# Optimization experiments

Measured on AMD Instinct MI355X. Metric: run time of the kernel, lower is better.

## Reference

```python
import jax, jax.numpy as jnp
import numpy as np

B, T, H, NCLS = 1024, 128, 512, 10
EMB, NDIG = 2, 3  # hard-coded in the torch module


def setup_inputs() -> dict:
    key = jax.random.key(0)
    ks = jax.random.split(key, 8)
    # kaiming_normal_ for a (fan_out, fan_in) matrix: std = sqrt(2/fan_in)
    def kaiming(k, shape):
        fan_in = shape[-1]
        return jax.random.normal(k, shape, dtype=jnp.float32) * np.sqrt(2.0 / fan_in)
    x = jax.random.randint(ks[0], (B, T), 0, NDIG)
    emb = jax.random.normal(ks[1], (NDIG, EMB), dtype=jnp.float32)
    # gate weights stacked in order (g, i, f, o) -> one fused GEMM per step
    Wx = jnp.concatenate([kaiming(ks[2 + j], (H, EMB)) for j in range(4)], axis=0)  # (4H, 2)
    kh = jax.random.split(ks[6], 4)
    Wh = jnp.concatenate([kaiming(kh[j], (H, H)) for j in range(4)], axis=0)  # (4H, H)
    b = jnp.zeros((4 * H,), dtype=jnp.float32)
    kp = jax.random.split(ks[7], 1)[0]
    Wp = kaiming(kp, (NCLS, H)).T  # stored transposed, as in the torch code
    bp = jnp.zeros((NCLS,), dtype=jnp.float32)
    return {"x": x, "emb": emb, "Wx": Wx, "Wh": Wh, "b": b, "Wp": Wp, "bp": bp}


def reference(x, emb, Wx, Wh, b, Wp, bp):
    # x: (B, T) int indices; emb: (3, 2); Wx: (4H, 2); Wh: (4H, H); b: (4H,)
    Bsz = x.shape[0]
    Hdim = Wh.shape[1]
    xe = emb[x]                                   # (B, T, 2) embedding lookup
    # precompute input projections for all timesteps (dim_x is tiny)
    gx_all = jnp.einsum('bte,ge->tbg', xe, Wx) + b  # (T, B, 4H)

    def step(carry, gx):
        h, c = carry
        z = gx + h @ Wh.T                         # (B, 4H) fused gate pre-activations
        g, i, f, o = jnp.split(z, 4, axis=-1)
        g = jnp.tanh(g)
        i = jax.nn.sigmoid(i)
        f = jax.nn.sigmoid(f)
        o = jax.nn.sigmoid(o)
        c = g * i + c * f
        h = jnp.tanh(c) * o
        return (h, c), None

    h0 = jnp.zeros((Bsz, Hdim), dtype=emb.dtype)
    c0 = jnp.zeros((Bsz, Hdim), dtype=emb.dtype)
    (h, _), _ = jax.lax.scan(step, (h0, c0), gx_all)
    p = h @ Wp + bp                               # only the last timestep's p is used
    return jax.nn.log_softmax(p, axis=-1)
```

## Files before the change

### kernel.cpp

```cpp
#include <hip/hip_runtime.h>
#include <math.h>

#define Bsz  1024
#define Tlen 128
#define Hdim 512
#define NCLS 10
#define NDIG 3
#define G4   2048

typedef short s8v __attribute__((ext_vector_type(8)));
typedef float f16v __attribute__((ext_vector_type(16)));

#define W6_OFF  0
#define GXD_OFF (2*1024*1024)
#define LL_OFF  (GXD_OFF + 32*1024)
#define LLF_OFF (LL_OFF + 4*1024*1024)
#define LLBUF   262144ull
#define WS_FAST_NEED ((size_t)LLF_OFF + 4*1024*1024)

static __device__ __forceinline__ unsigned short f2bf(float f) {
    unsigned int u = __float_as_uint(f);
    u = (u + 0x7FFFu + ((u >> 16) & 1u)) >> 16;
    return (unsigned short)u;
}
static __device__ __forceinline__ float bf2f(unsigned short s) {
    return __uint_as_float(((unsigned int)s) << 16);
}
static __device__ __forceinline__ s8v u2s(uint4 v) {
    union { uint4 u; s8v s; } x; x.u = v; return x.s;
}

__global__ __launch_bounds__(256) void prep_w6(const float* __restrict__ Wh,
                                               unsigned short* __restrict__ W6) {
    int idx = blockIdx.x * 256 + threadIdx.x;
    int l  = idx & 63;
    int c  = idx >> 6;
    int ks = c & 31, wn = c >> 5;
    int n  = wn * 32 + (l & 31);
    int jp = n >> 2, g = n & 3;
    int row = g * Hdim + jp;
    int kb  = ks * 16 + (l >> 5) * 8;
    const float* src = &Wh[(size_t)row * Hdim + kb];
    unsigned int p0 = f2bf(src[0]) | ((unsigned int)f2bf(src[1]) << 16);
    unsigned int p1 = f2bf(src[2]) | ((unsigned int)f2bf(src[3]) << 16);
    unsigned int p2 = f2bf(src[4]) | ((unsigned int)f2bf(src[5]) << 16);
    unsigned int p3 = f2bf(src[6]) | ((unsigned int)f2bf(src[7]) << 16);
    ((uint4*)W6)[idx] = make_uint4(p0, p1, p2, p3);
}

__global__ __launch_bounds__(256) void prep_gxd(const float* __restrict__ emb,
                                                const float* __restrict__ Wx,
                                                const float* __restrict__ b,
                                                float* __restrict__ gxd) {
    int idx = blockIdx.x * 256 + threadIdx.x;
    if (idx >= NDIG * G4) return;
    int col = idx % G4;
    int d   = idx / G4;
    int jp  = col >> 2;
    int g   = col & 3;
    int row = g * Hdim + jp;
    gxd[idx] = emb[d * 2 + 0] * Wx[row * 2 + 0]
             + emb[d * 2 + 1] * Wx[row * 2 + 1]
             + b[row];
}

__global__ __launch_bounds__(256) void zero_state(float4* __restrict__ p, int n4) {
    int i = blockIdx.x * 256 + threadIdx.x;
    if (i < n4) p[i] = make_float4(0.f, 0.f, 0.f, 0.f);
}

static __device__ __forceinline__ int slow_round(
    const unsigned long long* lr, unsigned int* hl, unsigned int want)
{
    unsigned long long g[16];
#pragma unroll
    for (int i = 0; i < 16; i++)
        g[i] = __hip_atomic_load(lr + i * 64, __ATOMIC_RELAXED,
                                 __HIP_MEMORY_SCOPE_AGENT);
    int ok = 1;
#pragma unroll
    for (int i = 0; i < 16; i++)
        ok &= ((unsigned int)(g[i] >> 32) == want) ? 1 : 0;
    if (!__all(ok)) return 0;
#pragma unroll
    for (int i = 0; i < 16; i++) hl[i * 64] = (unsigned int)g[i];
    return 1;
}

static __device__ __forceinline__ int try_fast(
    const unsigned long long* lr, unsigned int* hl, unsigned int want,
    int rounds)
{
    const unsigned long long* lrb = lr + 512;
    for (int r = 0; r < rounds; ++r) {
        unsigned long long g0,g1,g2,g3,g4,g5,g6,g7,g8,g9,g10,g11,g12,g13,g14,g15;
        asm volatile(
            "global_load_dwordx2 %[g0],  %[a], off sc0\n\t"
            "global_load_dwordx2 %[g1],  %[a], off offset:512 sc0\n\t"
            "global_load_dwordx2 %[g2],  %[a], off offset:1024 sc0\n\t"
            "global_load_dwordx2 %[g3],  %[a], off offset:1536 sc0\n\t"
            "global_load_dwordx2 %[g4],  %[a], off offset:2048 sc0\n\t"
            "global_load_dwordx2 %[g5],  %[a], off offset:2560 sc0\n\t"
            "global_load_dwordx2 %[g6],  %[a], off offset:3072 sc0\n\t"
            "global_load_dwordx2 %[g7],  %[a], off offset:3584 sc0\n\t"
            "global_load_dwordx2 %[g8],  %[b], off sc0\n\t"
            "global_load_dwordx2 %[g9],  %[b], off offset:512 sc0\n\t"
            "global_load_dwordx2 %[g10], %[b], off offset:1024 sc0\n\t"
            "global_load_dwordx2 %[g11], %[b], off offset:1536 sc0\n\t"
            "global_load_dwordx2 %[g12], %[b], off offset:2048 sc0\n\t"
            "global_load_dwordx2 %[g13], %[b], off offset:2560 sc0\n\t"
            "global_load_dwordx2 %[g14], %[b], off offset:3072 sc0\n\t"
            "global_load_dwordx2 %[g15], %[b], off offset:3584 sc0\n\t"
            "s_waitcnt vmcnt(0)"
            : [g0]"=&v"(g0),[g1]"=&v"(g1),[g2]"=&v"(g2),[g3]"=&v"(g3),
              [g4]"=&v"(g4),[g5]"=&v"(g5),[g6]"=&v"(g6),[g7]"=&v"(g7),
              [g8]"=&v"(g8),[g9]"=&v"(g9),[g10]"=&v"(g10),[g11]"=&v"(g11),
              [g12]"=&v"(g12),[g13]"=&v"(g13),[g14]"=&v"(g14),[g15]"=&v"(g15)
            : [a]"v"(lr), [b]"v"(lrb)
            : "memory");
        int ok = ((unsigned int)(g0  >> 32) == want) & ((unsigned int)(g1  >> 32) == want)
               & ((unsigned int)(g2  >> 32) == want) & ((unsigned int)(g3  >> 32) == want)
               & ((unsigned int)(g4  >> 32) == want) & ((unsigned int)(g5  >> 32) == want)
               & ((unsigned int)(g6  >> 32) == want) & ((unsigned int)(g7  >> 32) == want)
               & ((unsigned int)(g8  >> 32) == want) & ((unsigned int)(g9  >> 32) == want)
               & ((unsigned int)(g10 >> 32) == want) & ((unsigned int)(g11 >> 32) == want)
               & ((unsigned int)(g12 >> 32) == want) & ((unsigned int)(g13 >> 32) == want)
               & ((unsigned int)(g14 >> 32) == want) & ((unsigned int)(g15 >> 32) == want);
        if (__all(ok)) {
            hl[0*64]=(unsigned int)g0;   hl[1*64]=(unsigned int)g1;
            hl[2*64]=(unsigned int)g2;   hl[3*64]=(unsigned int)g3;
            hl[4*64]=(unsigned int)g4;   hl[5*64]=(unsigned int)g5;
            hl[6*64]=(unsigned int)g6;   hl[7*64]=(unsigned int)g7;
            hl[8*64]=(unsigned int)g8;   hl[9*64]=(unsigned int)g9;
            hl[10*64]=(unsigned int)g10; hl[11*64]=(unsigned int)g11;
            hl[12*64]=(unsigned int)g12; hl[13*64]=(unsigned int)g13;
            hl[14*64]=(unsigned int)g14; hl[15*64]=(unsigned int)g15;
            return 1;
        }
        if (r >= 2) __builtin_amdgcn_s_sleep(1);
    }
    return 0;
}

static __device__ __forceinline__ void stage_slice(
    const unsigned long long* fl, const unsigned long long* sl,
    unsigned int* hl, unsigned int want, int fasten, int burst)
{
    if (fasten && try_fast(fl, hl, want, burst)) return;
    for (;;) {
        if (slow_round(sl, hl, want)) return;
        if (fasten && try_fast(fl, hl, want, 1)) return;
        __builtin_amdgcn_s_sleep(1);
    }
}

__global__ __launch_bounds__(512, 2) void lstm_persist(
    const uint4* __restrict__ W6, const float* __restrict__ gxd,
    const int* __restrict__ x, unsigned long long* __restrict__ ll,
    unsigned long long* __restrict__ llf, int fasten,
    const float* __restrict__ Wp, const float* __restrict__ bp,
    float* __restrict__ out)
{
    __shared__ uint4 h_lds[2][2048];
    __shared__ float gxd_s[NDIG * G4];
    __shared__ int   x_s[4096];

    const int tid  = threadIdx.x;
    const int w    = tid >> 6;
    const int lane = tid & 63;
    const int hi   = lane >> 5;
    const int bl   = lane & 31;
    const int mt   = blockIdx.x & 31;
    const int nt   = blockIdx.x >> 5;

    s8v wfrag[32];
    {
        const uint4* wq = W6 + (size_t)((nt * 8 + w) * 32) * 64 + lane;
#pragma unroll
        for (int ks = 0; ks < 32; ks++) wfrag[ks] = u2s(wq[ks * 64]);
    }
    for (int i = tid; i < 4096; i += 512) {
        int b2 = i & 31, tt = i >> 5;
        x_s[tt * 32 + b2] = x[(mt * 32 + b2) * Tlen + tt];
    }
    for (int i = tid; i < NDIG * G4; i += 512) gxd_s[i] = gxd[i];
    __syncthreads();

    float c0 = 0.f, c1 = 0.f, c2 = 0.f, c3 = 0.f;
    const int jbase = nt * 64 + w * 8 + hi;
    const int q = (nt * 4 + (w >> 1)) * 64 + (w & 1) * 32 + bl;
    unsigned long long*       llst  = ll  + (size_t)mt * 8192 + q * 4 + hi * 2;
    unsigned long long*       llstf = llf + (size_t)mt * 8192 + q * 4 + hi * 2;
    const unsigned long long* llld  = ll  + (size_t)mt * 8192 + w * 1024 + lane;
    const unsigned long long* llfld = llf + (size_t)mt * 8192 + w * 1024 + lane;
    unsigned int* hlb = (unsigned int*)h_lds;

#pragma unroll 1
    for (int t = 0; t < Tlen; t++) {
        const int par = t & 1;

        stage_slice(llfld + (size_t)par * LLBUF, llld + (size_t)par * LLBUF,
                    hlb + par * 8192 + w * 1024 + lane, (unsigned int)t,
                    fasten, 8);
        __syncthreads();

        f16v acc = {0,0,0,0,0,0,0,0,0,0,0,0,0,0,0,0};
        const uint4* hb = &h_lds[par][0];
#pragma unroll
        for (int ks = 0; ks < 32; ks++) {
            s8v hf = u2s(hb[ks * 64 + lane]);
            acc = __builtin_amdgcn_mfma_f32_32x32x16_bf16(wfrag[ks], hf, acc,
                                                          0, 0, 0);
        }

        {
            int d = x_s[t * 32 + bl];
            float cc[4] = {c0, c1, c2, c3};
            unsigned short hh[4];
#pragma unroll
            for (int u = 0; u < 4; u++) {
                int jp = jbase + 2 * u;
                float4 g4 = *(const float4*)&gxd_s[d * G4 + jp * 4];
                float zg = acc[4*u+0] + g4.x;
                float zi = acc[4*u+1] + g4.y;
                float zf = acc[4*u+2] + g4.z;
                float zo = acc[4*u+3] + g4.w;
                float gv = 1.f - 2.f / (__expf(2.f * zg) + 1.f);
                float iv = 1.f / (1.f + __expf(-zi));
                float fv = 1.f / (1.f + __expf(-zf));
                float ov = 1.f / (1.f + __expf(-zo));
                float cn = gv * iv + cc[u] * fv;
                cc[u] = cn;
                hh[u] = f2bf((1.f - 2.f / (__expf(2.f * cn) + 1.f)) * ov);
            }
            c0 = cc[0]; c1 = cc[1]; c2 = cc[2]; c3 = cc[3];
            unsigned int p01 = (unsigned int)hh[0] | ((unsigned int)hh[1] << 16);
            unsigned int p23 = (unsigned int)hh[2] | ((unsigned int)hh[3] << 16);
            unsigned int q01 = __shfl_xor(p01, 32);
            unsigned int q23 = __shfl_xor(p23, 32);
            unsigned int lo2, hi2;
            if (hi == 0) {
                lo2 = (p01 & 0xffffu) | ((q01 & 0xffffu) << 16);
                hi2 = (p01 >> 16) | (q01 & 0xffff0000u);
            } else {
                lo2 = (q23 & 0xffffu) | ((p23 & 0xffffu) << 16);
                hi2 = (q23 >> 16) | (p23 & 0xffff0000u);
            }
            const unsigned long long tg =
                ((unsigned long long)(unsigned int)(t + 1)) << 32;
            const unsigned long long v0 = (unsigned long long)lo2 | tg;
            const unsigned long long v1 = (unsigned long long)hi2 | tg;
            const size_t pofs = (size_t)((t + 1) & 1) * LLBUF;
            if (fasten) {
                unsigned long long* fw = llstf + pofs;
                fw[0] = v0;
                fw[1] = v1;
            }
            unsigned long long* lw = llst + pofs;
            __hip_atomic_store(lw,     v0, __ATOMIC_RELAXED,
                               __HIP_MEMORY_SCOPE_AGENT);
            __hip_atomic_store(lw + 1, v1, __ATOMIC_RELAXED,
                               __HIP_MEMORY_SCOPE_AGENT);
        }
    }

    if (nt != 0) return;
    stage_slice(llfld, llld, hlb + w * 1024 + lane, (unsigned int)Tlen,
                fasten, 32);
    __syncthreads();
    float* wp_s = gxd_s;
    for (int i = tid; i < Hdim * NCLS; i += 512) wp_s[i] = Wp[i];
    __syncthreads();

#pragma unroll
    for (int rr = 0; rr < 4; rr++) {
        int blr = w * 4 + rr;
        int b   = mt * 32 + blr;
        uint4 hq = h_lds[0][(lane >> 1) * 64 + (lane & 1) * 32 + blr];
        union { uint4 u; unsigned short s[8]; } hu; hu.u = hq;
        float a[NCLS];
#pragma unroll
        for (int c = 0; c < NCLS; c++) a[c] = 0.f;
#pragma unroll
        for (int j = 0; j < 8; j++) {
            int k = lane * 8 + j;
            float hvv = bf2f(hu.s[j]);
#pragma unroll
            for (int c = 0; c < NCLS; c++) a[c] += hvv * wp_s[k * NCLS + c];
        }
#pragma unroll
        for (int off = 32; off > 0; off >>= 1) {
#pragma unroll
            for (int c = 0; c < NCLS; c++) a[c] += __shfl_down(a[c], off);
        }
        if (lane == 0) {
            float p[NCLS], m = -1e30f;
#pragma unroll
            for (int c = 0; c < NCLS; c++) { p[c] = a[c] + bp[c]; m = fmaxf(m, p[c]); }
            float s = 0.f;
#pragma unroll
            for (int c = 0; c < NCLS; c++) s += __expf(p[c] - m);
            float lse = m + logf(s);
#pragma unroll
            for (int c = 0; c < NCLS; c++) out[b * NCLS + c] = p[c] - lse;
        }
    }
}

extern "C" void kernel_launch(void* const* d_in, const int* in_sizes, int n_in,
                              void* d_out, int out_size, void* d_ws, size_t ws_size,
                              hipStream_t stream) {
    const int*   x   = (const int*)d_in[0];
    const float* emb = (const float*)d_in[1];
    const float* Wx  = (const float*)d_in[2];
    const float* Wh  = (const float*)d_in[3];
    const float* b   = (const float*)d_in[4];
    const float* Wp  = (const float*)d_in[5];
    const float* bp  = (const float*)d_in[6];
    float* out = (float*)d_out;
    char*  ws  = (char*)d_ws;

    int fasten = (ws_size >= WS_FAST_NEED) ? 1 : 0;

    unsigned short*     W6  = (unsigned short*)(ws + W6_OFF);
    float*              gxd = (float*)(ws + GXD_OFF);
    unsigned long long* ll  = (unsigned long long*)(ws + LL_OFF);
    unsigned long long* llf = (unsigned long long*)(ws + (fasten ? LLF_OFF
                                                                 : LL_OFF));

    prep_w6<<<512, 256, 0, stream>>>(Wh, W6);
    prep_gxd<<<(NDIG * G4 + 255) / 256, 256, 0, stream>>>(emb, Wx, b, gxd);
    {
        int nbytes = (fasten ? 8 : 4) * 1024 * 1024;
        int n4 = nbytes / 16;
        zero_state<<<(n4 + 255) / 256, 256, 0, stream>>>(
            (float4*)(ws + LL_OFF), n4);
    }

    void* args[] = { (void*)&W6, (void*)&gxd, (void*)&x, (void*)&ll,
                     (void*)&llf, (void*)&fasten,
                     (void*)&Wp, (void*)&bp, (void*)&out };
    hipLaunchCooperativeKernel((void*)lstm_persist, dim3(256), dim3(512),
                               args, 0, stream);
}
```

Baseline: 637.4 us.

## Add per-block sentinel flags to poll before reading fast h-exchange buffers

Adds a small sentinel array in the workspace. After writing its h slice to the fast buffer, each producer block waits for its stores to drain, runs a block barrier, and has thread 0 publish the step number. Consumers poll one sentinel word per producer before reading the full tagged slice, so they stop repeatedly loading the whole buffer. The cost is an extra vmcnt wait and __syncthreads per step on the producer side, plus the risk that sentinel visibility comes later than the data, which adds latency to the serial recurrence.

```diff
diff --git a/kernel.cpp b/kernel.cpp
--- a/kernel.cpp
+++ b/kernel.cpp
@@ -15,8 +15,9 @@
 #define GXD_OFF (2*1024*1024)
 #define LL_OFF  (GXD_OFF + 32*1024)
 #define LLF_OFF (LL_OFF + 4*1024*1024)
+#define SENT_OFF (LLF_OFF + 4*1024*1024)
 #define LLBUF   262144ull
-#define WS_FAST_NEED ((size_t)LLF_OFF + 4*1024*1024)
+#define WS_FAST_NEED ((size_t)SENT_OFF + 32*1024)
 
 static __device__ __forceinline__ unsigned short f2bf(float f) {
     unsigned int u = __float_as_uint(f);
@@ -144,9 +145,23 @@
 
 static __device__ __forceinline__ void stage_slice(
     const unsigned long long* fl, const unsigned long long* sl,
-    unsigned int* hl, unsigned int want, int fasten, int burst)
+    const unsigned int* sp, unsigned int* hl, unsigned int want,
+    int fasten, int burst)
 {
-    if (fasten && try_fast(fl, hl, want, burst)) return;
+    if (fasten) {
+        for (int r = 0; r < 64; ++r) {
+            unsigned int sv;
+            asm volatile("global_load_dword %0, %1, off sc0\n\t"
+                         "s_waitcnt vmcnt(0)"
+                         : "=&v"(sv) : "v"(sp) : "memory");
+            __builtin_amdgcn_sched_barrier(0);
+            if (__all((int)(sv == want))) {
+                if (try_fast(fl, hl, want, 1)) return;
+            }
+            if (r >= 4) __builtin_amdgcn_s_sleep(1);
+        }
+        if (try_fast(fl, hl, want, burst)) return;
+    }
     for (;;) {
         if (slow_round(sl, hl, want)) return;
         if (fasten && try_fast(fl, hl, want, 1)) return;
@@ -193,6 +208,9 @@
     unsigned long long*       llstf = llf + (size_t)mt * 8192 + q * 4 + hi * 2;
     const unsigned long long* llld  = ll  + (size_t)mt * 8192 + w * 1024 + lane;
     const unsigned long long* llfld = llf + (size_t)mt * 8192 + w * 1024 + lane;
+    unsigned int* sent = (unsigned int*)((char*)llf + 4*1024*1024);
+    const unsigned int* sprd = sent + (mt * 8 + w) * 16;
+    volatile unsigned int* spub = sent + (mt * 8 + nt) * 16;
     unsigned int* hlb = (unsigned int*)h_lds;
 
 #pragma unroll 1
@@ -200,6 +218,7 @@
         const int par = t & 1;
 
         stage_slice(llfld + (size_t)par * LLBUF, llld + (size_t)par * LLBUF,
+                    sprd + par * 4096,
                     hlb + par * 8192 + w * 1024 + lane, (unsigned int)t,
                     fasten, 8);
         __syncthreads();
@@ -256,6 +275,9 @@
                 fw[0] = v0;
                 fw[1] = v1;
             }
+            asm volatile("s_waitcnt vmcnt(0)" ::: "memory");
+            __syncthreads();
+            if (fasten && tid == 0) spub[((t + 1) & 1) * 4096] = t + 1;
             unsigned long long* lw = llst + pofs;
             __hip_atomic_store(lw,     v0, __ATOMIC_RELAXED,
                                __HIP_MEMORY_SCOPE_AGENT);
@@ -265,7 +287,7 @@
     }
 
     if (nt != 0) return;
-    stage_slice(llfld, llld, hlb + w * 1024 + lane, (unsigned int)Tlen,
+    stage_slice(llfld, llld, sprd, hlb + w * 1024 + lane, (unsigned int)Tlen,
                 fasten, 32);
     __syncthreads();
     float* wp_s = gxd_s;
@@ -331,7 +353,7 @@
     prep_w6<<<512, 256, 0, stream>>>(Wh, W6);
     prep_gxd<<<(NDIG * G4 + 255) / 256, 256, 0, stream>>>(emb, Wx, b, gxd);
     {
-        int nbytes = (fasten ? 8 : 4) * 1024 * 1024;
+        int nbytes = fasten ? (8 * 1024 * 1024 + 32 * 1024) : (4 * 1024 * 1024);
         int n4 = nbytes / 16;
         zero_state<<<(n4 + 255) / 256, 256, 0, stream>>>(
             (float4*)(ws + LL_OFF), n4);
```

Result: slower. 1.326 ms (+108.1%).

## Write own h slice to LDS directly, skip self polling, split MFMA chains

Applied to the files above, without the earlier changes.

Each block now writes its own freshly computed h slice straight into the next LDS h buffer and skips polling global memory for that slice (warp w == nt). This removes a round trip through the global flag buffer for local data. The MFMA reduction is split into two independent accumulator chains to shorten the dependent latency. The gate-bias loads are hoisted ahead of the matmul. The risk lies in the correctness of the index mapping between the local slice and the staging warp, and in the extra registers used by the second accumulator.

```diff
diff --git a/kernel.cpp b/kernel.cpp
--- a/kernel.cpp
+++ b/kernel.cpp
@@ -184,6 +184,7 @@
         x_s[tt * 32 + b2] = x[(mt * 32 + b2) * Tlen + tt];
     }
     for (int i = tid; i < NDIG * G4; i += 512) gxd_s[i] = gxd[i];
+    for (int i = tid; i < 2048; i += 512) h_lds[0][i] = make_uint4(0, 0, 0, 0);
     __syncthreads();
 
     float c0 = 0.f, c1 = 0.f, c2 = 0.f, c3 = 0.f;
@@ -199,32 +200,41 @@
     for (int t = 0; t < Tlen; t++) {
         const int par = t & 1;
 
-        stage_slice(llfld + (size_t)par * LLBUF, llld + (size_t)par * LLBUF,
-                    hlb + par * 8192 + w * 1024 + lane, (unsigned int)t,
-                    fasten, 8);
+        if (w != nt)
+            stage_slice(llfld + (size_t)par * LLBUF, llld + (size_t)par * LLBUF,
+                        hlb + par * 8192 + w * 1024 + lane, (unsigned int)t,
+                        fasten, 8);
         __syncthreads();
 
-        f16v acc = {0,0,0,0,0,0,0,0,0,0,0,0,0,0,0,0};
+        int d = x_s[t * 32 + bl];
+        float4 g4p[4];
+#pragma unroll
+        for (int u = 0; u < 4; u++)
+            g4p[u] = *(const float4*)&gxd_s[d * G4 + (jbase + 2 * u) * 4];
+
+        f16v acc0 = {0,0,0,0,0,0,0,0,0,0,0,0,0,0,0,0};
+        f16v acc1 = {0,0,0,0,0,0,0,0,0,0,0,0,0,0,0,0};
         const uint4* hb = &h_lds[par][0];
 #pragma unroll
-        for (int ks = 0; ks < 32; ks++) {
-            s8v hf = u2s(hb[ks * 64 + lane]);
-            acc = __builtin_amdgcn_mfma_f32_32x32x16_bf16(wfrag[ks], hf, acc,
-                                                          0, 0, 0);
-        }
+        for (int ks = 0; ks < 16; ks++) {
+            s8v hf0 = u2s(hb[ks * 64 + lane]);
+            s8v hf1 = u2s(hb[(ks + 16) * 64 + lane]);
+            acc0 = __builtin_amdgcn_mfma_f32_32x32x16_bf16(wfrag[ks], hf0, acc0,
+                                                           0, 0, 0);
+            acc1 = __builtin_amdgcn_mfma_f32_32x32x16_bf16(wfrag[ks + 16], hf1,
+                                                           acc1, 0, 0, 0);
+        }
+        f16v acc = acc0 + acc1;
 
         {
-            int d = x_s[t * 32 + bl];
             float cc[4] = {c0, c1, c2, c3};
             unsigned short hh[4];
 #pragma unroll
             for (int u = 0; u < 4; u++) {
-                int jp = jbase + 2 * u;
-                float4 g4 = *(const float4*)&gxd_s[d * G4 + jp * 4];
-                float zg = acc[4*u+0] + g4.x;
-                float zi = acc[4*u+1] + g4.y;
-                float zf = acc[4*u+2] + g4.z;
-                float zo = acc[4*u+3] + g4.w;
+                float zg = acc[4*u+0] + g4p[u].x;
+                float zi = acc[4*u+1] + g4p[u].y;
+                float zf = acc[4*u+2] + g4p[u].z;
+                float zo = acc[4*u+3] + g4p[u].w;
                 float gv = 1.f - 2.f / (__expf(2.f * zg) + 1.f);
                 float iv = 1.f / (1.f + __expf(-zi));
                 float fv = 1.f / (1.f + __expf(-zf));
@@ -246,6 +256,8 @@
                 lo2 = (q23 & 0xffffu) | ((p23 & 0xffffu) << 16);
                 hi2 = (q23 >> 16) | (p23 & 0xffff0000u);
             }
+            *(unsigned long long*)&hlb[((t + 1) & 1) * 8192 + q * 4 + hi * 2] =
+                ((unsigned long long)hi2 << 32) | (unsigned long long)lo2;
             const unsigned long long tg =
                 ((unsigned long long)(unsigned int)(t + 1)) << 32;
             const unsigned long long v0 = (unsigned long long)lo2 | tg;
@@ -265,8 +277,9 @@
     }
 
     if (nt != 0) return;
-    stage_slice(llfld, llld, hlb + w * 1024 + lane, (unsigned int)Tlen,
-                fasten, 32);
+    if (w != 0)
+        stage_slice(llfld, llld, hlb + w * 1024 + lane, (unsigned int)Tlen,
+                    fasten, 32);
     __syncthreads();
     float* wp_s = gxd_s;
     for (int i = tid; i < Hdim * NCLS; i += 512) wp_s[i] = Wp[i];
```

Result: slower. 794.0 us (+24.6%).
